# Performance work log

Measured on AMD Instinct MI355X. Metric: run time of the kernel, lower is better.

## Reference

```python
import jax, jax.numpy as jnp
import numpy as np

N_NODES = 100000
N_EDGES = 1600000
N_GRAPHS = 1024
EMB = 32
HID = 64
N_CLASSES = 10
N_SHAPE = 16
N_COLOR = 8


def setup_inputs() -> dict:
    key = jax.random.key(0)
    ks = jax.random.split(key, 12)
    shape_id = jax.random.randint(ks[0], (N_NODES,), 0, N_SHAPE + 1, dtype=jnp.int32)
    color_id = jax.random.randint(ks[1], (N_NODES,), 0, N_COLOR + 1, dtype=jnp.int32)
    edge_index = jax.random.randint(ks[2], (2, N_EDGES), 0, N_NODES, dtype=jnp.int32)
    batch = jnp.sort(jax.random.randint(ks[3], (N_NODES,), 0, N_GRAPHS, dtype=jnp.int32))
    shape_table = jax.random.normal(ks[4], (N_SHAPE + 1, EMB), jnp.float32)
    color_table = jax.random.normal(ks[5], (N_COLOR + 1, EMB), jnp.float32)
    W1 = jax.random.normal(ks[6], (EMB, HID), jnp.float32) / np.sqrt(EMB)
    b1 = jnp.zeros((HID,), jnp.float32)
    W2 = jax.random.normal(ks[7], (HID, HID), jnp.float32) / np.sqrt(HID)
    b2 = jnp.zeros((HID,), jnp.float32)
    Wl = jax.random.normal(ks[8], (HID, N_CLASSES), jnp.float32) / np.sqrt(HID)
    bl = jnp.zeros((N_CLASSES,), jnp.float32)
    return dict(shape_id=shape_id, color_id=color_id, edge_index=edge_index, batch=batch,
                shape_table=shape_table, color_table=color_table,
                W1=W1, b1=b1, W2=W2, b2=b2, Wl=Wl, bl=bl)


def gcn_conv(x, W, b, src, dst, num_nodes):
    # PyG GCNConv: add self-loops, symmetric normalization D^-1/2 (A+I) D^-1/2
    h = x @ W  # [N, out]
    deg = 1.0 + jax.ops.segment_sum(jnp.ones_like(dst, jnp.float32), dst, num_segments=num_nodes)
    dis = jax.lax.rsqrt(deg)  # deg >= 1 due to self-loop
    norm = dis[src] * dis[dst]  # [E]
    agg = jax.ops.segment_sum(h[src] * norm[:, None], dst, num_segments=num_nodes)
    agg = agg + h * (dis * dis)[:, None]  # self-loop term
    return agg + b


def reference(shape_id, color_id, edge_index, batch, shape_table, color_table,
              W1, b1, W2, b2, Wl, bl):
    # padding_idx=0 -> row 0 contributes zeros
    st = shape_table.at[0].set(0.0)
    ct = color_table.at[0].set(0.0)
    x = st[shape_id] + ct[color_id]  # [N, emb]
    src, dst = edge_index[0], edge_index[1]
    x = jax.nn.relu(gcn_conv(x, W1, b1, src, dst, N_NODES))
    x = jax.nn.relu(gcn_conv(x, W2, b2, src, dst, N_NODES))
    # global_mean_pool over batch ids
    sums = jax.ops.segment_sum(x, batch, num_segments=N_GRAPHS)
    cnts = jax.ops.segment_sum(jnp.ones((x.shape[0],), x.dtype), batch, num_segments=N_GRAPHS)
    pooled = sums / jnp.maximum(cnts, 1.0)[:, None]  # [B, hidden]
    return pooled @ Wl + bl  # [B, num_classes]
```

## Files before the change

### kernel.cpp

```cpp
#include <hip/hip_runtime.h>
#include <hip/hip_bf16.h>
#include <hip/hip_fp16.h>

#define N_NODES   100000
#define N_EDGES   1600000
#define N_GRAPHS  1024
#define EMB       32
#define HID       64
#define N_CLASSES 10
#define SCAN_BLOCKS 391
#define NCOMBO 153
#define BUCK_NODES 448
#define NBUCK 224
#define BIN_CAP 8192
#define EPB 4096
#define PBCAP 11328
#define SENTINEL N_NODES

typedef _Float16 f16x8 __attribute__((ext_vector_type(8)));
typedef float f32x4 __attribute__((ext_vector_type(4)));

__global__ __launch_bounds__(256) void prep_kernel(
    const int* __restrict__ sid, const int* __restrict__ cid,
    const int* __restrict__ batch, int* __restrict__ combo, int* __restrict__ gstart,
    const float* __restrict__ st, const float* __restrict__ ct,
    const float* __restrict__ W1, __half* __restrict__ TCh,
    float* __restrict__ pooled, int* __restrict__ gcur, __half* __restrict__ h2s) {
    int t = threadIdx.x;
    int v = blockIdx.x * 256 + t;
    if (v < N_GRAPHS * HID) pooled[v] = 0.0f;
    if (blockIdx.x == 0) {
        if (t < NBUCK) gcur[t] = 0;
        if (t == 0) combo[N_NODES] = 0;
        if (t < 32) ((float*)(h2s + (size_t)N_NODES * HID))[t] = 0.0f;
    }
    if (v < N_NODES) {
        combo[v] = sid[v] * 9 + cid[v];
        int b = batch[v];
        int bp = (v == 0) ? -1 : batch[v - 1];
        for (int g = bp + 1; g <= b; ++g) gstart[g] = v;
        if (v == N_NODES - 1) {
            for (int g = b + 1; g <= N_GRAPHS; ++g) gstart[g] = N_NODES;
        }
    }
    if (blockIdx.x < NCOMBO && t >= 64 && t < 128) {
        int r = blockIdx.x, j = t - 64;
        int s = r / 9, c = r % 9;
        float acc = 0.0f;
        if (s != 0) {
#pragma unroll
            for (int k = 0; k < EMB; ++k) acc = fmaf(st[s * EMB + k], W1[k * HID + j], acc);
        }
        if (c != 0) {
#pragma unroll
            for (int k = 0; k < EMB; ++k) acc = fmaf(ct[c * EMB + k], W1[k * HID + j], acc);
        }
        TCh[r * HID + j] = __float2half_rn(acc);
    }
}

__global__ __launch_bounds__(512) void binA_kernel(
    const int* __restrict__ src, const int* __restrict__ dst,
    int* __restrict__ gcur, int* __restrict__ gbin) {
    __shared__ int2 stg[EPB];
    __shared__ int hist[NBUCK];
    __shared__ int base[NBUCK + 1];
    __shared__ int gstart[NBUCK];
    __shared__ int scanbuf[256];
    int t = threadIdx.x;
    int e0 = blockIdx.x * EPB;
    for (int i = t; i < NBUCK; i += 512) hist[i] = 0;
    __syncthreads();

    int2 myq[8];
    int mybo[8];
    if (e0 + EPB <= N_EDGES) {
        int eb = e0 + t * 8;
        int4 sa4 = *(const int4*)&src[eb];
        int4 sb4 = *(const int4*)&src[eb + 4];
        int4 da4 = *(const int4*)&dst[eb];
        int4 db4 = *(const int4*)&dst[eb + 4];
        int ss[8] = {sa4.x, sa4.y, sa4.z, sa4.w, sb4.x, sb4.y, sb4.z, sb4.w};
        int dd[8] = {da4.x, da4.y, da4.z, da4.w, db4.x, db4.y, db4.z, db4.w};
#pragma unroll
        for (int i = 0; i < 8; ++i) {
            unsigned b = (unsigned)dd[i] / BUCK_NODES;
            int off = atomicAdd(&hist[b], 1);
            myq[i].x = ss[i];
            myq[i].y = dd[i];
            mybo[i] = (int)(b << 16) | off;
        }
    } else {
#pragma unroll
        for (int i = 0; i < 8; ++i) {
            int e = e0 + t * 8 + i;
            if (e < N_EDGES) {
                int d = dst[e];
                unsigned b = (unsigned)d / BUCK_NODES;
                int off = atomicAdd(&hist[b], 1);
                myq[i].x = src[e];
                myq[i].y = d;
                mybo[i] = (int)(b << 16) | off;
            } else {
                mybo[i] = -1;
            }
        }
    }
    __syncthreads();

    int h = (t < NBUCK) ? hist[t] : 0;
    if (t < 256) scanbuf[t] = h;
    __syncthreads();
#pragma unroll
    for (int off = 1; off < 256; off <<= 1) {
        int x = (t < 256 && t >= off) ? scanbuf[t - off] : 0;
        __syncthreads();
        if (t < 256) scanbuf[t] += x;
        __syncthreads();
    }
    if (t < NBUCK) base[t] = scanbuf[t] - h;
    if (t == 0) base[NBUCK] = scanbuf[255];
    __syncthreads();
#pragma unroll
    for (int i = 0; i < 8; ++i) {
        if (mybo[i] >= 0) {
            int b = mybo[i] >> 16, off = mybo[i] & 0xFFFF;
            stg[base[b] + off] = myq[i];
        }
    }
    if (t < NBUCK) {
        int n = hist[t];
        gstart[t] = n ? atomicAdd(&gcur[t], n) : 0;
    }
    __syncthreads();
    int total = base[NBUCK];
    for (int i = t; i < total; i += 512) {
        int2 q = stg[i];
        unsigned b = (unsigned)q.y / BUCK_NODES;
        int local = q.y - (int)b * BUCK_NODES;
        gbin[(size_t)b * BIN_CAP + gstart[b] + (i - base[b])] = q.x | (local << 17);
    }
}

__global__ __launch_bounds__(1024) void bucket_scatter_kernel(
    const int* __restrict__ gbin, const int* __restrict__ gcur,
    float* __restrict__ dis, int* __restrict__ rowptr, int* __restrict__ epack4) {
    __shared__ __align__(16) int pbin[BIN_CAP];
    __shared__ int ldeg[BUCK_NODES];
    __shared__ int rbase[BUCK_NODES];
    __shared__ int s[512];
    int b = blockIdx.x, t = threadIdx.x;
    for (int i = t; i < BUCK_NODES; i += 1024) ldeg[i] = 0;
    __syncthreads();
    int n = gcur[b];
    int nc = (n + 3) >> 2;
    {
        const int4* my4 = (const int4*)(gbin + (size_t)b * BIN_CAP);
        for (int c = t; c < nc; c += 1024) {
            int4 p4 = my4[c];
            ((int4*)pbin)[c] = p4;
            int i0 = c * 4;
            if (i0 + 0 < n) atomicAdd(&ldeg[(unsigned)p4.x >> 17], 1);
            if (i0 + 1 < n) atomicAdd(&ldeg[(unsigned)p4.y >> 17], 1);
            if (i0 + 2 < n) atomicAdd(&ldeg[(unsigned)p4.z >> 17], 1);
            if (i0 + 3 < n) atomicAdd(&ldeg[(unsigned)p4.w >> 17], 1);
        }
    }
    __syncthreads();
    int d = (t < BUCK_NODES) ? ldeg[t] : 0;
    int v = b * BUCK_NODES + t;
    if (t < BUCK_NODES && v < N_NODES) dis[v] = rsqrtf(1.0f + (float)d);
    if (b == 0 && t == 0) dis[N_NODES] = 0.0f;
    int dp = (d + 7) & ~7;
    if (dp > 248) dp = 248;
    if (t < 512) s[t] = dp;
    __syncthreads();
#pragma unroll
    for (int off = 1; off < 512; off <<= 1) {
        int x = (t < 512 && t >= off) ? s[t - off] : 0;
        __syncthreads();
        if (t < 512) s[t] += x;
        __syncthreads();
    }
    int rp = 0;
    if (t < 512) rp = b * PBCAP + s[t] - dp;
    if (t < BUCK_NODES) {
        rbase[t] = rp;
        if (v < N_NODES) rowptr[v] = rp | (dp << 24);
    }
    for (int i = t; i < BUCK_NODES; i += 1024) ldeg[i] = 0;
    __syncthreads();
    if (t < BUCK_NODES) {
        for (int k = d; k < dp; ++k) epack4[rp + k] = SENTINEL;
    }
    for (int i = t; i < n; i += 1024) {
        int p = pbin[i];
        int local = (unsigned)p >> 17;
        int r = atomicAdd(&ldeg[local], 1);
        if (r < 248) epack4[rbase[local] + r] = p & 0x1FFFF;
    }
}

#define AGG_CHUNK(CQ, DQ, LBASE)                                               \
    _Pragma("unroll")                                                          \
    for (int i = 0; i < 8; ++i) {                                              \
        int off = __builtin_amdgcn_readlane((CQ), (LBASE) + i);                \
        int wb  = __builtin_amdgcn_readlane(__float_as_int(DQ), (LBASE) + i);  \
        __half tv = *(const __half*)((const char*)TCs + (off + lane2));        \
        acc = fmaf(__int_as_float(wb), __half2float(tv), acc);                 \
    }

#define AGG_NODE(N, RP, DEG, DV, CO)                                           \
    {                                                                          \
        int deg = (DEG);                                                       \
        int cnt = deg > 32 ? 32 : deg;                                         \
        float acc = 0.0f;                                                      \
        if (cnt > 0)  { AGG_CHUNK(cq1, dq1, (N)*16) }                          \
        if (cnt > 8)  { AGG_CHUNK(cq1, dq1, (N)*16 + 8) }                      \
        if (cnt > 16) { AGG_CHUNK(cq2, dq2, (N)*16) }                          \
        if (cnt > 24) { AGG_CHUNK(cq2, dq2, (N)*16 + 8) }                      \
        if (deg > 32) {                                                        \
            for (int e = (RP) + 32; e < (RP) + deg; ++e) {                     \
                int qx = epack4[e] & 0x1FFFF;                                  \
                float dw = dis[qx];                                            \
                __half tv = *(const __half*)((const char*)TCs +                \
                                             ((combo[qx] << 7) + lane2));      \
                acc = fmaf(dw, __half2float(tv), acc);                         \
            }                                                                  \
        }                                                                      \
        __half hv = *(const __half*)((const char*)TCs + ((CO) + lane2));       \
        float val = (DV) * fmaf(__half2float(hv), (DV), acc) + bias;           \
        val = val > 0.0f ? val : 0.0f;                                         \
        xsA[w * 4 + (N)][lane] = __float2half_rn(val * (DV));                  \
    }

__global__ __launch_bounds__(256, 8) void agg1_mm2_kernel(
    const int* __restrict__ epack4, const int* __restrict__ rowptr,
    const int* __restrict__ combo, const float* __restrict__ dis,
    const __half* __restrict__ TCh, const float* __restrict__ W2,
    const float* __restrict__ b1, __half* __restrict__ h2s) {
    __shared__ __align__(16) __half TCs[NCOMBO * HID];
    __shared__ __align__(16) __half xsA[16][72];
    int t = threadIdx.x;
    int lane = t & 63, w = t >> 6;
    int lane2 = lane * 2;
    int vb = blockIdx.x * 16;
    int v0 = vb + w * 4;

    int sub = lane >> 4, sl = lane & 15;
    int rb = rowptr[v0 + sub] & 0xFFFFFF;
    int q1x = epack4[rb + sl] & 0x1FFFF;
    int q2x = epack4[rb + 16 + sl] & 0x1FFFF;
    float dq1 = dis[q1x];
    float dq2 = dis[q2x];
    int cq1 = combo[q1x] << 7;
    int cq2 = combo[q2x] << 7;

    int r0p = __builtin_amdgcn_readfirstlane(rowptr[v0]);
    int r1p = __builtin_amdgcn_readfirstlane(rowptr[v0 + 1]);
    int r2p = __builtin_amdgcn_readfirstlane(rowptr[v0 + 2]);
    int r3p = __builtin_amdgcn_readfirstlane(rowptr[v0 + 3]);
    int r0 = r0p & 0xFFFFFF, g0 = (int)((unsigned)r0p >> 24);
    int r1 = r1p & 0xFFFFFF, g1 = (int)((unsigned)r1p >> 24);
    int r2 = r2p & 0xFFFFFF, g2 = (int)((unsigned)r2p >> 24);
    int r3 = r3p & 0xFFFFFF, g3 = (int)((unsigned)r3p >> 24);

    float d0 = dis[v0], d1 = dis[v0 + 1], d2 = dis[v0 + 2], d3 = dis[v0 + 3];
    int o0 = combo[v0] << 7, o1 = combo[v0 + 1] << 7;
    int o2 = combo[v0 + 2] << 7, o3 = combo[v0 + 3] << 7;
    float bias = b1[lane];

    f16x8 bf0, bf1;
    {
        int colw = (w << 4) + (lane & 15);
        int kb = (lane >> 4) * 8;
#pragma unroll
        for (int i = 0; i < 8; ++i) {
            bf0[i] = (_Float16)W2[(kb + i) * HID + colw];
            bf1[i] = (_Float16)W2[(32 + kb + i) * HID + colw];
        }
    }

    {
        const int4* s4 = (const int4*)TCh;
        int4* dd4 = (int4*)TCs;
        for (int i = t; i < NCOMBO * HID * 2 / 16; i += 256) dd4[i] = s4[i];
    }
    __syncthreads();

    AGG_NODE(0, r0, g0, d0, o0)
    AGG_NODE(1, r1, g1, d1, o1)
    AGG_NODE(2, r2, g2, d2, o2)
    AGG_NODE(3, r3, g3, d3, o3)

    __syncthreads();

    const __half* xa = &xsA[lane & 15][0];
    f16x8 a0 = *(const f16x8*)(xa + (lane >> 4) * 8);
    f16x8 a1 = *(const f16x8*)(xa + 32 + (lane >> 4) * 8);
    __syncthreads();
    f32x4 dacc = {0.0f, 0.0f, 0.0f, 0.0f};
    dacc = __builtin_amdgcn_mfma_f32_16x16x32_f16(a0, bf0, dacc, 0, 0, 0);
    dacc = __builtin_amdgcn_mfma_f32_16x16x32_f16(a1, bf1, dacc, 0, 0, 0);

    __half* Dst = (__half*)xsA;
    {
        int colg = (w << 4) + (lane & 15);
#pragma unroll
        for (int i = 0; i < 4; ++i)
            Dst[((lane >> 4) * 4 + i) * 64 + colg] = __float2half_rn(dacc[i]);
    }
    __syncthreads();

    {
        const uint2* ds2 = (const uint2*)Dst;
        uint2* go = (uint2*)(h2s + (size_t)vb * HID);
        go[t] = ds2[t];
    }
}

__device__ __forceinline__ float agg2_node(const int* __restrict__ epack4, int sx,
                                           int rs, int deg, int lane, int lane2,
                                           const __half* __restrict__ h2s) {
    float acc = 0.0f;
    int p = rs;
    int re = rs + deg;
    for (;;) {
        int avail = re - p;
        int cnt = avail > 64 ? 64 : avail;
        int vo = sx << 7;
        for (int j = 0; j + 8 <= cnt; j += 8) {
            float g[8];
#pragma unroll
            for (int i = 0; i < 8; ++i) {
                int off = __builtin_amdgcn_readlane(vo, j + i);
                g[i] = __half2float(*(const __half*)((const char*)h2s + (off + lane2)));
            }
#pragma unroll
            for (int i = 0; i < 8; ++i) acc += g[i];
        }
        p += 64;
        if (p >= re) break;
        sx = epack4[p + lane];
    }
    return acc;
}

__global__ __launch_bounds__(256, 8) void agg2_pool_kernel(
    const int* __restrict__ epack4, const int* __restrict__ rowptr,
    const __half* __restrict__ h2s, const float* __restrict__ dis,
    const float* __restrict__ b2, const int* __restrict__ batch,
    float* __restrict__ pooled) {
    int t = threadIdx.x, lane = t & 63, w = t >> 6;
    int lane2 = lane * 2;
    int v0 = (blockIdx.x * 4 + w) * 4;

    int r0p = __builtin_amdgcn_readfirstlane(rowptr[v0]);
    int r1p = __builtin_amdgcn_readfirstlane(rowptr[v0 + 1]);
    int r2p = __builtin_amdgcn_readfirstlane(rowptr[v0 + 2]);
    int r3p = __builtin_amdgcn_readfirstlane(rowptr[v0 + 3]);
    int r0 = r0p & 0xFFFFFF, dp0 = (int)((unsigned)r0p >> 24);
    int r1 = r1p & 0xFFFFFF, dp1 = (int)((unsigned)r1p >> 24);
    int r2 = r2p & 0xFFFFFF, dp2 = (int)((unsigned)r2p >> 24);
    int r3 = r3p & 0xFFFFFF, dp3 = (int)((unsigned)r3p >> 24);

    int sa = epack4[r0 + lane];
    int sb = epack4[r1 + lane];
    int sc = epack4[r2 + lane];
    int sd = epack4[r3 + lane];

    float bv = b2[lane];
    float acc0 = agg2_node(epack4, sa, r0, dp0, lane, lane2, h2s);
    float acc1 = agg2_node(epack4, sb, r1, dp1, lane, lane2, h2s);
    float acc2 = agg2_node(epack4, sc, r2, dp2, lane, lane2, h2s);
    float acc3 = agg2_node(epack4, sd, r3, dp3, lane, lane2, h2s);

#define AGG2_VAL(V, ACC, OUT)                                                  \
    {                                                                          \
        float dv = dis[V];                                                     \
        float self = __half2float(h2s[(size_t)(V) * HID + lane]);              \
        float val = dv * ((ACC) + self) + bv;                                  \
        OUT = val > 0.0f ? val : 0.0f;                                         \
    }
    float val0, val1, val2, val3;
    AGG2_VAL(v0, acc0, val0)
    AGG2_VAL(v0 + 1, acc1, val1)
    AGG2_VAL(v0 + 2, acc2, val2)
    AGG2_VAL(v0 + 3, acc3, val3)
#undef AGG2_VAL

    int g0 = __builtin_amdgcn_readfirstlane(batch[v0]);
    int g1 = __builtin_amdgcn_readfirstlane(batch[v0 + 1]);
    int g2 = __builtin_amdgcn_readfirstlane(batch[v0 + 2]);
    int g3 = __builtin_amdgcn_readfirstlane(batch[v0 + 3]);
    float s = val0; int g = g0;
    if (g1 == g) { s += val1; } else { unsafeAtomicAdd(&pooled[g * HID + lane], s); g = g1; s = val1; }
    if (g2 == g) { s += val2; } else { unsafeAtomicAdd(&pooled[g * HID + lane], s); g = g2; s = val2; }
    if (g3 == g) { s += val3; } else { unsafeAtomicAdd(&pooled[g * HID + lane], s); g = g3; s = val3; }
    unsafeAtomicAdd(&pooled[g * HID + lane], s);
}

__global__ __launch_bounds__(64) void logits_kernel(
    const float* __restrict__ pooled, const int* __restrict__ gstart,
    const float* __restrict__ Wl, const float* __restrict__ bl,
    float* __restrict__ out) {
    __shared__ float row[HID];
    int g = blockIdx.x, t = threadIdx.x;
    int c = gstart[g + 1] - gstart[g]; if (c < 1) c = 1;
    row[t] = pooled[g * HID + t] / (float)c;
    __syncthreads();
    if (t < N_CLASSES) {
        float acc = bl[t];
#pragma unroll
        for (int k = 0; k < HID; ++k) acc = fmaf(row[k], Wl[k * N_CLASSES + t], acc);
        out[g * N_CLASSES + t] = acc;
    }
}

extern "C" void kernel_launch(void* const* d_in, const int* in_sizes, int n_in,
                              void* d_out, int out_size, void* d_ws, size_t ws_size,
                              hipStream_t stream) {
    const int*   shape_id = (const int*)d_in[0];
    const int*   color_id = (const int*)d_in[1];
    const int*   edge_idx = (const int*)d_in[2];
    const int*   batch    = (const int*)d_in[3];
    const float* st       = (const float*)d_in[4];
    const float* ct       = (const float*)d_in[5];
    const float* W1       = (const float*)d_in[6];
    const float* b1       = (const float*)d_in[7];
    const float* W2       = (const float*)d_in[8];
    const float* b2       = (const float*)d_in[9];
    const float* Wl       = (const float*)d_in[10];
    const float* bl       = (const float*)d_in[11];
    float* out = (float*)d_out;

    const int* src = edge_idx;
    const int* dst = edge_idx + N_EDGES;

    char* ws = (char*)d_ws;
    int*    combo   = (int*)   (ws + 0);
    float*  dis     = (float*) (ws + 400384);
    int*    gstart  = (int*)   (ws + 801792);
    int*    rowptr  = (int*)   (ws + 1201152);
    __half* TCh     = (__half*)(ws + 1603584);
    float*  pooled  = (float*) (ws + 1623552);
    int*    gcur    = (int*)   (ws + 1889792);
    int*    epack4  = (int*)   (ws + 1890816);
    int*    gbin    = (int*)   (ws + 14690816);
    __half* h2s     = (__half*)(ws + 29370880);

    prep_kernel<<<SCAN_BLOCKS, 256, 0, stream>>>(shape_id, color_id, batch, combo, gstart,
                                                 st, ct, W1, TCh, pooled, gcur, h2s);

    binA_kernel<<<(N_EDGES + EPB - 1) / EPB, 512, 0, stream>>>(src, dst, gcur, gbin);

    bucket_scatter_kernel<<<NBUCK, 1024, 0, stream>>>(gbin, gcur, dis, rowptr, epack4);

    agg1_mm2_kernel<<<6250, 256, 0, stream>>>(epack4, rowptr, combo, dis, TCh, W2, b1, h2s);

    agg2_pool_kernel<<<6250, 256, 0, stream>>>(epack4, rowptr, h2s, dis, b2, batch, pooled);

    logits_kernel<<<N_GRAPHS, 64, 0, stream>>>(pooled, gstart, Wl, bl, out);
}
```

Baseline: 179.5 us.

## Make agg1 kernel persistent over two tiles with prefetch, unroll agg2 gathers by 16

The agg1_mm2 kernel now launches half as many blocks, and each block loops over two 16-node tiles. While it aggregates the current tile, it prefetches the next tile's rowptr, neighbour indices, dis and combo values. This also amortises the per-block staging of the TC table into LDS and the W2 fragment loads across two tiles. Launch bounds drop to 7 blocks per SM to leave room for the extra registers. Separately, the agg2 gather loop issues 16 half loads per iteration instead of 8, with an 8-wide tail, to raise memory-level parallelism.

Result: no change. 176.1 us (-1.9%).

```diff
diff --git a/kernel.cpp b/kernel.cpp
--- a/kernel.cpp
+++ b/kernel.cpp
@@ -16,6 +16,8 @@
 #define EPB 4096
 #define PBCAP 11328
 #define SENTINEL N_NODES
+#define NTILES 6250
+#define AGG_GRID 3125
 
 typedef _Float16 f16x8 __attribute__((ext_vector_type(8)));
 typedef float f32x4 __attribute__((ext_vector_type(4)));
@@ -234,7 +236,7 @@
         xsA[w * 4 + (N)][lane] = __float2half_rn(val * (DV));                  \
     }
 
-__global__ __launch_bounds__(256, 8) void agg1_mm2_kernel(
+__global__ __launch_bounds__(256, 7) void agg1_mm2_kernel(
     const int* __restrict__ epack4, const int* __restrict__ rowptr,
     const int* __restrict__ combo, const float* __restrict__ dis,
     const __half* __restrict__ TCh, const float* __restrict__ W2,
@@ -244,32 +246,26 @@
     int t = threadIdx.x;
     int lane = t & 63, w = t >> 6;
     int lane2 = lane * 2;
-    int vb = blockIdx.x * 16;
-    int v0 = vb + w * 4;
-
     int sub = lane >> 4, sl = lane & 15;
+
+    int tile = blockIdx.x;
+    int v0 = tile * 16 + w * 4;
+    {
+    }
     int rb = rowptr[v0 + sub] & 0xFFFFFF;
     int q1x = epack4[rb + sl] & 0x1FFFF;
     int q2x = epack4[rb + 16 + sl] & 0x1FFFF;
-    float dq1 = dis[q1x];
-    float dq2 = dis[q2x];
-    int cq1 = combo[q1x] << 7;
-    int cq2 = combo[q2x] << 7;
-
+    float dq1 = dis[q1x], dq2 = dis[q2x];
+    int cq1 = combo[q1x] << 7, cq2 = combo[q2x] << 7;
     int r0p = __builtin_amdgcn_readfirstlane(rowptr[v0]);
     int r1p = __builtin_amdgcn_readfirstlane(rowptr[v0 + 1]);
     int r2p = __builtin_amdgcn_readfirstlane(rowptr[v0 + 2]);
     int r3p = __builtin_amdgcn_readfirstlane(rowptr[v0 + 3]);
-    int r0 = r0p & 0xFFFFFF, g0 = (int)((unsigned)r0p >> 24);
-    int r1 = r1p & 0xFFFFFF, g1 = (int)((unsigned)r1p >> 24);
-    int r2 = r2p & 0xFFFFFF, g2 = (int)((unsigned)r2p >> 24);
-    int r3 = r3p & 0xFFFFFF, g3 = (int)((unsigned)r3p >> 24);
-
     float d0 = dis[v0], d1 = dis[v0 + 1], d2 = dis[v0 + 2], d3 = dis[v0 + 3];
     int o0 = combo[v0] << 7, o1 = combo[v0 + 1] << 7;
     int o2 = combo[v0 + 2] << 7, o3 = combo[v0 + 3] << 7;
+
     float bias = b1[lane];
-
     f16x8 bf0, bf1;
     {
         int colw = (w << 4) + (lane & 15);
@@ -280,7 +276,6 @@
             bf1[i] = (_Float16)W2[(32 + kb + i) * HID + colw];
         }
     }
-
     {
         const int4* s4 = (const int4*)TCh;
         int4* dd4 = (int4*)TCs;
@@ -288,34 +283,67 @@
     }
     __syncthreads();
 
-    AGG_NODE(0, r0, g0, d0, o0)
-    AGG_NODE(1, r1, g1, d1, o1)
-    AGG_NODE(2, r2, g2, d2, o2)
-    AGG_NODE(3, r3, g3, d3, o3)
-
-    __syncthreads();
-
-    const __half* xa = &xsA[lane & 15][0];
-    f16x8 a0 = *(const f16x8*)(xa + (lane >> 4) * 8);
-    f16x8 a1 = *(const f16x8*)(xa + 32 + (lane >> 4) * 8);
-    __syncthreads();
-    f32x4 dacc = {0.0f, 0.0f, 0.0f, 0.0f};
-    dacc = __builtin_amdgcn_mfma_f32_16x16x32_f16(a0, bf0, dacc, 0, 0, 0);
-    dacc = __builtin_amdgcn_mfma_f32_16x16x32_f16(a1, bf1, dacc, 0, 0, 0);
-
-    __half* Dst = (__half*)xsA;
-    {
-        int colg = (w << 4) + (lane & 15);
-#pragma unroll
-        for (int i = 0; i < 4; ++i)
-            Dst[((lane >> 4) * 4 + i) * 64 + colg] = __float2half_rn(dacc[i]);
-    }
-    __syncthreads();
-
-    {
-        const uint2* ds2 = (const uint2*)Dst;
-        uint2* go = (uint2*)(h2s + (size_t)vb * HID);
-        go[t] = ds2[t];
+    for (;;) {
+        int ntile = tile + AGG_GRID;
+        bool more = ntile < NTILES;
+        int nv0 = 0, nq1x = 0, nq2x = 0;
+        int nr0p = 0, nr1p = 0, nr2p = 0, nr3p = 0;
+        float ndq1 = 0.0f, ndq2 = 0.0f, nd0 = 0.0f, nd1 = 0.0f, nd2 = 0.0f, nd3 = 0.0f;
+        int ncq1 = 0, ncq2 = 0, no0 = 0, no1 = 0, no2 = 0, no3 = 0;
+        if (more) {
+            nv0 = ntile * 16 + w * 4;
+            int nrb = rowptr[nv0 + sub] & 0xFFFFFF;
+            nq1x = epack4[nrb + sl] & 0x1FFFF;
+            nq2x = epack4[nrb + 16 + sl] & 0x1FFFF;
+            ndq1 = dis[nq1x]; ndq2 = dis[nq2x];
+            ncq1 = combo[nq1x] << 7; ncq2 = combo[nq2x] << 7;
+            nr0p = __builtin_amdgcn_readfirstlane(rowptr[nv0]);
+            nr1p = __builtin_amdgcn_readfirstlane(rowptr[nv0 + 1]);
+            nr2p = __builtin_amdgcn_readfirstlane(rowptr[nv0 + 2]);
+            nr3p = __builtin_amdgcn_readfirstlane(rowptr[nv0 + 3]);
+            nd0 = dis[nv0]; nd1 = dis[nv0 + 1]; nd2 = dis[nv0 + 2]; nd3 = dis[nv0 + 3];
+            no0 = combo[nv0] << 7; no1 = combo[nv0 + 1] << 7;
+            no2 = combo[nv0 + 2] << 7; no3 = combo[nv0 + 3] << 7;
+        }
+        int r0 = r0p & 0xFFFFFF, g0 = (int)((unsigned)r0p >> 24);
+        int r1 = r1p & 0xFFFFFF, g1 = (int)((unsigned)r1p >> 24);
+        int r2 = r2p & 0xFFFFFF, g2 = (int)((unsigned)r2p >> 24);
+        int r3 = r3p & 0xFFFFFF, g3 = (int)((unsigned)r3p >> 24);
+        AGG_NODE(0, r0, g0, d0, o0)
+        AGG_NODE(1, r1, g1, d1, o1)
+        AGG_NODE(2, r2, g2, d2, o2)
+        AGG_NODE(3, r3, g3, d3, o3)
+        __syncthreads();
+
+        const __half* xa = &xsA[lane & 15][0];
+        f16x8 a0 = *(const f16x8*)(xa + (lane >> 4) * 8);
+        f16x8 a1 = *(const f16x8*)(xa + 32 + (lane >> 4) * 8);
+        __syncthreads();
+        f32x4 dacc = {0.0f, 0.0f, 0.0f, 0.0f};
+        dacc = __builtin_amdgcn_mfma_f32_16x16x32_f16(a0, bf0, dacc, 0, 0, 0);
+        dacc = __builtin_amdgcn_mfma_f32_16x16x32_f16(a1, bf1, dacc, 0, 0, 0);
+
+        __half* Dst = (__half*)xsA;
+        {
+            int colg = (w << 4) + (lane & 15);
+#pragma unroll
+            for (int i = 0; i < 4; ++i)
+                Dst[((lane >> 4) * 4 + i) * 64 + colg] = __float2half_rn(dacc[i]);
+        }
+        __syncthreads();
+
+        {
+            const uint2* ds2 = (const uint2*)Dst;
+            uint2* go = (uint2*)(h2s + (size_t)tile * 16 * HID);
+            go[t] = ds2[t];
+        }
+        if (!more) break;
+        __syncthreads();
+        tile = ntile; v0 = nv0;
+        q1x = nq1x; q2x = nq2x; dq1 = ndq1; dq2 = ndq2; cq1 = ncq1; cq2 = ncq2;
+        r0p = nr0p; r1p = nr1p; r2p = nr2p; r3p = nr3p;
+        d0 = nd0; d1 = nd1; d2 = nd2; d3 = nd3;
+        o0 = no0; o1 = no1; o2 = no2; o3 = no3;
     }
 }
 
@@ -329,7 +357,18 @@
         int avail = re - p;
         int cnt = avail > 64 ? 64 : avail;
         int vo = sx << 7;
-        for (int j = 0; j + 8 <= cnt; j += 8) {
+        int j = 0;
+        for (; j + 16 <= cnt; j += 16) {
+            float g[16];
+#pragma unroll
+            for (int i = 0; i < 16; ++i) {
+                int off = __builtin_amdgcn_readlane(vo, j + i);
+                g[i] = __half2float(*(const __half*)((const char*)h2s + (off + lane2)));
+            }
+#pragma unroll
+            for (int i = 0; i < 16; ++i) acc += g[i];
+        }
+        if (j < cnt) {
             float g[8];
 #pragma unroll
             for (int i = 0; i < 8; ++i) {
@@ -456,7 +495,7 @@
 
     bucket_scatter_kernel<<<NBUCK, 1024, 0, stream>>>(gbin, gcur, dis, rowptr, epack4);
 
-    agg1_mm2_kernel<<<6250, 256, 0, stream>>>(epack4, rowptr, combo, dis, TCh, W2, b1, h2s);
+    agg1_mm2_kernel<<<AGG_GRID, 256, 0, stream>>>(epack4, rowptr, combo, dis, TCh, W2, b1, h2s);
 
     agg2_pool_kernel<<<6250, 256, 0, stream>>>(epack4, rowptr, h2s, dis, b2, batch, pooled);
 
```
